# Optimization experiments

Hardware: AMD Instinct MI355X
Metric: run time of the kernel (lower is better)

Reference implementation:

```python
import jax, jax.numpy as jnp
import numpy as np

H = 4096        # hidden_size
NH = 32         # num query heads
NG = 8          # num query groups (kv heads)
HD = H // NH    # head size = 128
B, S = 2, 2048


def gen_rope_cache(seq_length, n_elem, base=10000.0):
    theta = 1.0 / base ** (jnp.arange(0, n_elem, 2, dtype=jnp.float32) / n_elem)
    idx_theta = jnp.outer(jnp.arange(seq_length, dtype=jnp.float32), theta)
    return jnp.stack([jnp.cos(idx_theta), jnp.sin(idx_theta)], axis=-1)  # [S, n_elem//2, 2]


def apply_rope(x, cache):
    # x: [B, S, nh, hd], cache: [S, hd//2, 2]; rot_dim == hd (no pass-through)
    b, s, nh, hd = x.shape
    xr = x.reshape(b, s, nh, hd // 2, 2)
    c = cache[:s].reshape(1, s, 1, hd // 2, 2)
    out = jnp.stack([
        xr[..., 0] * c[..., 0] - xr[..., 1] * c[..., 1],
        xr[..., 1] * c[..., 0] + xr[..., 0] * c[..., 1],
    ], axis=-1)
    return out.reshape(b, s, nh, hd)


def setup_inputs() -> dict:
    key = jax.random.key(0)
    k1, k2, k3, k4 = jax.random.split(key, 4)
    x = jax.random.normal(k1, (B, S, H), dtype=jnp.float32)
    W_qkv = jax.random.normal(k2, (H, H + 2 * NG * HD), dtype=jnp.float32) * 0.02
    b_qkv = jax.random.normal(k3, (H + 2 * NG * HD,), dtype=jnp.float32) * 0.02
    W_dense = jax.random.normal(k4, (H, H), dtype=jnp.float32) * 0.02
    rope_cache = gen_rope_cache(S, HD)
    return {"x": x, "rope_cache": rope_cache, "W_qkv": W_qkv, "b_qkv": b_qkv, "W_dense": W_dense}


def reference(x, rope_cache, W_qkv, b_qkv, W_dense):
    b, s, h = x.shape
    qkv = jnp.einsum('bsh,ho->bso', x, W_qkv) + b_qkv
    q, k, v = jnp.split(qkv, [h, h + NG * HD], axis=-1)
    q = q.reshape(b, s, NH, HD)
    k = k.reshape(b, s, NG, HD)
    v = v.reshape(b, s, NG, HD)
    q = apply_rope(q, rope_cache)
    k = apply_rope(k, rope_cache)
    # GQA: group query heads [B, G, rep, S, D] against kv [B, G, S, D]
    rep = NH // NG
    qg = q.transpose(0, 2, 1, 3).reshape(b, NG, rep, s, HD)
    kg = k.transpose(0, 2, 1, 3)  # [B, G, S, D]
    vg = v.transpose(0, 2, 1, 3)
    scale = 1.0 / jnp.sqrt(jnp.float32(HD))
    scores = jnp.einsum('bgrqd,bgkd->bgrqk', qg, kg) * scale
    causal = jnp.tril(jnp.ones((s, s), dtype=bool))
    scores = jnp.where(causal, scores, jnp.float32(-1e30))
    attn = jax.nn.softmax(scores, axis=-1)
    out = jnp.einsum('bgrqk,bgkd->bgrqd', attn, vg)  # [B, G, rep, S, D]
    out = out.reshape(b, NH, s, HD).transpose(0, 2, 1, 3).reshape(b, s, h)
    return jnp.einsum('bsh,ho->bso', out, W_dense)
```

## Files before the change

kernel.cpp:

```cpp
#include <hip/hip_runtime.h>
#include <hip/hip_bf16.h>
#include <math.h>

#define BS   4096
#define HH   4096
#define NH   32
#define NG   8
#define HD   128
#define SEQ  2048
#define NQKV 6144

typedef float f32x4 __attribute__((ext_vector_type(4)));
typedef float f32x16 __attribute__((ext_vector_type(16)));
typedef short s16x8 __attribute__((ext_vector_type(8)));
typedef short s16x4 __attribute__((ext_vector_type(4)));
typedef unsigned int u32x4 __attribute__((ext_vector_type(4)));

__device__ __forceinline__ unsigned short f2bf(float f) {
  unsigned int u = __builtin_bit_cast(unsigned int, f);
  unsigned int r = (u + 0x7fffu + ((u >> 16) & 1u)) >> 16;
  return (unsigned short)r;
}
__device__ __forceinline__ float b2f(short h) {
  unsigned int u = ((unsigned int)(unsigned short)h) << 16;
  return __builtin_bit_cast(float, u);
}

__device__ __forceinline__ void gload16(const void* g, void* l) {
  __builtin_amdgcn_global_load_lds((__attribute__((address_space(1))) void*)(g),
                                   (__attribute__((address_space(3))) void*)(l), 16, 0, 0);
}

#define BARRIER __builtin_amdgcn_s_barrier()
#define PRIO1 __builtin_amdgcn_s_setprio(1)
#define PRIO0 __builtin_amdgcn_s_setprio(0)

__global__ void cast_f32_bf16(const float* __restrict__ in, short* __restrict__ out, long n4) {
  long i = (long)blockIdx.x * blockDim.x + threadIdx.x;
  long stride = (long)gridDim.x * blockDim.x;
  for (; i < n4; i += stride) {
    float4 v = *(const float4*)&in[i * 4];
    s16x4 o;
    o[0] = (short)f2bf(v.x); o[1] = (short)f2bf(v.y);
    o[2] = (short)f2bf(v.z); o[3] = (short)f2bf(v.w);
    *(s16x4*)&out[i * 4] = o;
  }
}

__global__ __launch_bounds__(256) void transpose_cast(const float* __restrict__ in,
                                                      short* __restrict__ out, int R, int C) {
  __shared__ float tile[32][33];
  int tx = threadIdx.x & 31, ty = threadIdx.x >> 5;
  long c0 = (long)blockIdx.x * 32, r0 = (long)blockIdx.y * 32;
#pragma unroll
  for (int j = 0; j < 32; j += 8)
    tile[ty + j][tx] = in[(r0 + ty + j) * C + c0 + tx];
  __syncthreads();
#pragma unroll
  for (int j = 0; j < 32; j += 8)
    out[(c0 + ty + j) * R + r0 + tx] = (short)f2bf(tile[tx][ty + j]);
}

__global__ __launch_bounds__(256) void transpose_v(const short* __restrict__ in,
                                                   short* __restrict__ out) {
  __shared__ short tile[32][33];
  int tx = threadIdx.x & 31, ty = threadIdx.x >> 5;
  int head = blockIdx.x >> 8;
  int s0 = ((blockIdx.x >> 2) & 63) * 32;
  int d0 = (blockIdx.x & 3) * 32;
  const short* src = in + (long)head * SEQ * HD;
  short* dst = out + (long)head * SEQ * HD;
#pragma unroll
  for (int j = 0; j < 32; j += 8)
    tile[ty + j][tx] = src[(long)(s0 + ty + j) * HD + d0 + tx];
  __syncthreads();
#pragma unroll
  for (int j = 0; j < 32; j += 8)
    dst[(long)(d0 + ty + j) * SEQ + s0 + tx] = tile[tx][ty + j];
}

#define LDA_FR(BASE, DB)                                                         \
  {                                                                              \
    _Pragma("unroll") for (int mf = 0; mf < 4; ++mf)                             \
      _Pragma("unroll") for (int ks = 0; ks < 2; ++ks)                           \
        af[mf][ks] = *(const s16x8*)&lds[(BASE) + (DB) * 8192 + aoff[mf][ks]];   \
  }
#define LDB_FR(BASE, DB)                                                         \
  {                                                                              \
    _Pragma("unroll") for (int nf = 0; nf < 2; ++nf)                             \
      _Pragma("unroll") for (int ks = 0; ks < 2; ++ks)                           \
        bf[nf][ks] = *(const s16x8*)&lds[(BASE) + (DB) * 8192 + boff[nf][ks]];   \
  }
#define MF_Q(MS, NS)                                                             \
  {                                                                              \
    _Pragma("unroll") for (int ks = 0; ks < 2; ++ks)                             \
      _Pragma("unroll") for (int mf = 0; mf < 4; ++mf)                           \
        _Pragma("unroll") for (int nf = 0; nf < 2; ++nf)                         \
          acc[(MS) * 4 + mf][(NS) * 2 + nf] = __builtin_amdgcn_mfma_f32_16x16x32_bf16( \
              af[mf][ks], bf[nf][ks], acc[(MS) * 4 + mf][(NS) * 2 + nf], 0, 0, 0);     \
  }
#define STG_AU0(DB, KB) { gload16(sA0 + (KB), &lds[0 + (DB) * 8192 + du0]);            \
                          gload16(sA1 + (KB), &lds[0 + (DB) * 8192 + du1]); }
#define STG_BU0(DB, KB) { gload16(sB0 + (KB), &lds[32768 + (DB) * 8192 + du0]);        \
                          gload16(sB1 + (KB), &lds[32768 + (DB) * 8192 + du1]); }
#define STG_AU1(DB, KB) { gload16(sA0 + 64 * (long)K + (KB), &lds[16384 + (DB) * 8192 + du0]); \
                          gload16(sA1 + 64 * (long)K + (KB), &lds[16384 + (DB) * 8192 + du1]); }
#define STG_BU1(DB, KB) { gload16(sB0 + 32 * (long)K + (KB), &lds[49152 + (DB) * 8192 + du0]); \
                          gload16(sB1 + 32 * (long)K + (KB), &lds[49152 + (DB) * 8192 + du1]); }

#define TILE256(DB, KBS)                                                         \
  LDA_FR(0, DB); LDB_FR(32768, DB);                                              \
  STG_AU0(DB ^ 1, KBS); STG_BU0(DB ^ 1, KBS);                                    \
  BARRIER;                                                                       \
  PRIO1; MF_Q(0, 0); PRIO0;                                                      \
  asm volatile("s_waitcnt vmcnt(6)" ::: "memory");                               \
  BARRIER;                                                                       \
  LDA_FR(16384, DB);                                                             \
  STG_AU1(DB ^ 1, KBS);                                                          \
  BARRIER;                                                                       \
  PRIO1; MF_Q(1, 0); PRIO0;                                                      \
  asm volatile("s_waitcnt vmcnt(6)" ::: "memory");                               \
  BARRIER;                                                                       \
  LDB_FR(49152, DB);                                                             \
  STG_BU1(DB ^ 1, KBS);                                                          \
  BARRIER;                                                                       \
  PRIO1; MF_Q(1, 1); PRIO0;                                                      \
  BARRIER;                                                                       \
  LDA_FR(0, DB);                                                                 \
  BARRIER;                                                                       \
  PRIO1; MF_Q(0, 1); PRIO0;                                                      \
  asm volatile("s_waitcnt vmcnt(4)" ::: "memory");                               \
  BARRIER;

template <int OUT_BF16, int ADD_BIAS>
__global__ __launch_bounds__(512, 1) void gemm256(const short* __restrict__ A,
                                                  const short* __restrict__ Bt,
                                                  const float* __restrict__ bias,
                                                  void* __restrict__ Cout,
                                                  int M, int N, int K) {
  extern __shared__ short lds[];
  const int t = threadIdx.x;
  const int lane = t & 63, w = t >> 6;
  const int g = lane >> 4, lr = lane & 15;
  const int wm = w >> 2, wn = w & 3;
  const long bm = (long)blockIdx.y * 256;
  const long bn = (long)blockIdx.x * 256;

  const short *sA0, *sA1, *sB0, *sB1;
  {
    int c0 = t, c1 = t + 512;
    int h0 = c0 >> 9, r0 = (c0 >> 3) & 63, tc0 = (c0 & 7) ^ (r0 & 7);
    int h1 = c1 >> 9, r1 = (c1 >> 3) & 63, tc1 = (c1 & 7) ^ (r1 & 7);
    sA0 = A + (bm + h0 * 128 + r0) * (long)K + tc0 * 8;
    sA1 = A + (bm + h1 * 128 + r1) * (long)K + tc1 * 8;
    int g0 = c0 >> 8, rb0 = (c0 >> 3) & 31, tb0 = (c0 & 7) ^ (rb0 & 7);
    int g1 = c1 >> 8, rb1 = (c1 >> 3) & 31, tb1 = (c1 & 7) ^ (rb1 & 7);
    sB0 = Bt + (bn + g0 * 64 + rb0) * (long)K + tb0 * 8;
    sB1 = Bt + (bn + g1 * 64 + rb1) * (long)K + tb1 * 8;
  }
  const int du0 = w * 512;
  const int du1 = w * 512 + 4096;

  int aoff[4][2], boff[2][2];
#pragma unroll
  for (int mf = 0; mf < 4; ++mf)
#pragma unroll
    for (int ks = 0; ks < 2; ++ks)
      aoff[mf][ks] = wm * 4096 + (mf * 16 + lr) * 64 + (((ks * 4 + g) ^ (lr & 7)) * 8);
#pragma unroll
  for (int nf = 0; nf < 2; ++nf)
#pragma unroll
    for (int ks = 0; ks < 2; ++ks)
      boff[nf][ks] = wn * 2048 + (nf * 16 + lr) * 64 + (((ks * 4 + g) ^ (lr & 7)) * 8);

  f32x4 acc[8][4] = {};
  s16x8 af[4][2], bf[2][2];

  STG_AU0(0, 0); STG_BU0(0, 0); STG_AU1(0, 0); STG_BU1(0, 0);
  asm volatile("s_waitcnt vmcnt(0)" ::: "memory");
  BARRIER;

  const int NT = K >> 6;
  for (int kt = 0; kt < NT; kt += 2) {
    const long kb1 = (long)(kt + 1) * 64;
    const long kb2 = (kt + 2 < NT) ? (long)(kt + 2) * 64 : 0l;
    TILE256(0, kb1);
    TILE256(1, kb2);
  }

#pragma unroll
  for (int am = 0; am < 8; ++am) {
    long row = bm + wm * 128 + am * 16 + g * 4;
#pragma unroll
    for (int an = 0; an < 4; ++an) {
      long col = bn + wn * 64 + an * 16 + lr;
      float bv = ADD_BIAS ? bias[col] : 0.0f;
#pragma unroll
      for (int r = 0; r < 4; ++r) {
        float v = acc[am][an][r] + bv;
        if (OUT_BF16) ((short*)Cout)[(row + r) * N + col] = (short)f2bf(v);
        else          ((float*)Cout)[(row + r) * N + col] = v;
      }
    }
  }
}

__global__ void rope_split(const short* __restrict__ qkv, const float* __restrict__ cache,
                           short* __restrict__ Qb, short* __restrict__ Kb,
                           short* __restrict__ Vb) {
  long id = (long)blockIdx.x * blockDim.x + threadIdx.x;
  const long total = (long)BS * (NQKV / 4);
  if (id >= total) return;
  int c4 = (int)(id % (NQKV / 4));
  int row = (int)(id / (NQKV / 4));
  int s = row & (SEQ - 1);
  int b = row >> 11;
  int col = c4 * 4;
  s16x4 in = *(const s16x4*)&qkv[(long)row * NQKV + col];
  if (col < HH) {
    int h = col >> 7, d = col & 127;
    const float4 cs = *(const float4*)&cache[((long)s * 64 + (d >> 1)) * 2];
    float x0 = b2f(in[0]), x1 = b2f(in[1]), x2 = b2f(in[2]), x3 = b2f(in[3]);
    const float sc = 0.12751743f;
    s16x4 o;
    o[0] = (short)f2bf((x0 * cs.x - x1 * cs.y) * sc);
    o[1] = (short)f2bf((x1 * cs.x + x0 * cs.y) * sc);
    o[2] = (short)f2bf((x2 * cs.z - x3 * cs.w) * sc);
    o[3] = (short)f2bf((x3 * cs.z + x2 * cs.w) * sc);
    *(s16x4*)&Qb[(((long)(b * NH + h)) * SEQ + s) * HD + d] = o;
  } else if (col < HH + NG * HD) {
    int cc = col - HH;
    int gi = cc >> 7, d = cc & 127;
    const float4 cs = *(const float4*)&cache[((long)s * 64 + (d >> 1)) * 2];
    float x0 = b2f(in[0]), x1 = b2f(in[1]), x2 = b2f(in[2]), x3 = b2f(in[3]);
    s16x4 o;
    o[0] = (short)f2bf(x0 * cs.x - x1 * cs.y);
    o[1] = (short)f2bf(x1 * cs.x + x0 * cs.y);
    o[2] = (short)f2bf(x2 * cs.z - x3 * cs.w);
    o[3] = (short)f2bf(x3 * cs.z + x2 * cs.w);
    *(s16x4*)&Kb[(((long)(b * NG + gi)) * SEQ + s) * HD + d] = o;
  } else {
    int cc = col - HH - NG * HD;
    int gi = cc >> 7, d = cc & 127;
    *(s16x4*)&Vb[(((long)(b * NG + gi)) * SEQ + s) * HD + d] = in;
  }
}

__global__ __launch_bounds__(512, 1) void attn(const short* __restrict__ Qb,
                                               const short* __restrict__ Kb,
                                               const short* __restrict__ Vtb,
                                               short* __restrict__ Ob) {
  extern __shared__ short alds[];
  const int t = threadIdx.x, lane = t & 63, w = t >> 6;
  const int l31 = lane & 31, hi = lane >> 5;
  const int qt = 7 - (int)(blockIdx.x >> 6);
  const int head = blockIdx.x & 63;
  const int b = head >> 5, h = head & 31;
  const int qb = qt * 256;
  const short* Qhead = Qb + (long)(b * NH + h) * SEQ * HD;
  const short* Khead = Kb + (long)(b * NG + (h >> 2)) * SEQ * HD;
  const short* Vthead = Vtb + (long)(b * NG + (h >> 2)) * SEQ * HD;
  const int qw0 = qb + w * 32;
  const int qrow = qw0 + l31;
  float* facs = (float*)&alds[32768] + w * 32;

  s16x8 qf[8];
#pragma unroll
  for (int ds = 0; ds < 8; ++ds)
    qf[ds] = *(const s16x8*)&Qhead[(long)qrow * HD + ds * 16 + hi * 8];

  const short *kp0, *kp1, *vp0, *vp1;
  {
    int c0 = t, c1 = t + 512;
    int kr0 = c0 >> 4, kc0 = (c0 & 15) ^ (kr0 & 15);
    int kr1 = c1 >> 4, kc1 = (c1 & 15) ^ (kr1 & 15);
    kp0 = Khead + (long)kr0 * HD + kc0 * 8;
    kp1 = Khead + (long)kr1 * HD + kc1 * 8;
    int vr0 = c0 >> 3, vc0 = (c0 & 7) ^ (vr0 & 7);
    int vr1 = c1 >> 3, vc1 = (c1 & 7) ^ (vr1 & 7);
    vp0 = Vthead + (long)vr0 * SEQ + vc0 * 8;
    vp1 = Vthead + (long)vr1 * SEQ + vc1 * 8;
  }
  const int d0 = w * 512, d1 = w * 512 + 4096;

  f32x16 ao[4] = {};
  float mrun = -1.0e30f, lrun = 0.0f;
  const int nkt = 4 * qt + 4;

  gload16(kp0, &alds[d0]); gload16(kp1, &alds[d1]);
  gload16(vp0, &alds[16384 + d0]); gload16(vp1, &alds[16384 + d1]);
  kp0 += 64 * HD; kp1 += 64 * HD; vp0 += 64; vp1 += 64;
  asm volatile("s_waitcnt vmcnt(0)" ::: "memory");
  BARRIER;

  for (int kt = 0; kt < nkt; ++kt) {
    const int buf = kt & 1, nb = buf ^ 1;
    const int kb = kt * 64;
    const int bK = buf * 8192, bV = 16384 + buf * 8192;
    if (kt + 1 < nkt) {
      gload16(kp0, &alds[nb * 8192 + d0]); gload16(kp1, &alds[nb * 8192 + d1]);
      gload16(vp0, &alds[16384 + nb * 8192 + d0]); gload16(vp1, &alds[16384 + nb * 8192 + d1]);
      kp0 += 64 * HD; kp1 += 64 * HD; vp0 += 64; vp1 += 64;
    }
    if (kb <= qw0 + 31) {
      f32x16 st0 = {}, st1 = {};
      PRIO1;
#pragma unroll
      for (int ds = 0; ds < 8; ++ds) {
        const int c = ds * 2 + hi;
        const int r0 = l31, r1 = 32 + l31;
        s16x8 kf0 = *(const s16x8*)&alds[bK + r0 * 128 + ((c ^ (r0 & 15)) * 8)];
        s16x8 kf1 = *(const s16x8*)&alds[bK + r1 * 128 + ((c ^ (r1 & 15)) * 8)];
        st0 = __builtin_amdgcn_mfma_f32_32x32x16_bf16(kf0, qf[ds], st0, 0, 0, 0);
        st1 = __builtin_amdgcn_mfma_f32_32x32x16_bf16(kf1, qf[ds], st1, 0, 0, 0);
      }
      PRIO0;

      float p[32];
      if (kb + 63 > qrow || kb + 63 > qw0) {
#pragma unroll
        for (int r = 0; r < 16; ++r) {
          int kg = kb + (r & 3) + 8 * (r >> 2) + 4 * hi;
          p[r] = (kg > qrow) ? -1.0e30f : st0[r];
          p[16 + r] = (kg + 32 > qrow) ? -1.0e30f : st1[r];
        }
      } else {
#pragma unroll
        for (int r = 0; r < 16; ++r) { p[r] = st0[r]; p[16 + r] = st1[r]; }
      }
      float tmax = -1.0e30f;
#pragma unroll
      for (int i = 0; i < 32; ++i) tmax = fmaxf(tmax, p[i]);
      tmax = fmaxf(tmax, __shfl_xor(tmax, 32));
      if (!__all(tmax <= mrun + 8.0f)) {
        float mnew = fmaxf(mrun, tmax);
        float fac = exp2f(mrun - mnew);
        facs[l31] = fac;
        mrun = mnew; lrun *= fac;
        f32x4 f0 = *(f32x4*)&facs[0 + 4 * hi];
        f32x4 f1 = *(f32x4*)&facs[8 + 4 * hi];
        f32x4 f2 = *(f32x4*)&facs[16 + 4 * hi];
        f32x4 f3 = *(f32x4*)&facs[24 + 4 * hi];
#pragma unroll
        for (int j = 0; j < 4; ++j)
#pragma unroll
          for (int dt = 0; dt < 4; ++dt) {
            ao[dt][j] *= f0[j]; ao[dt][4 + j] *= f1[j];
            ao[dt][8 + j] *= f2[j]; ao[dt][12 + j] *= f3[j];
          }
      }
      float tsum = 0.0f;
#pragma unroll
      for (int i = 0; i < 32; ++i) { p[i] = exp2f(p[i] - mrun); tsum += p[i]; }
      lrun += tsum + __shfl_xor(tsum, 32);

      s16x8 pa[4];
#pragma unroll
      for (int ks = 0; ks < 4; ++ks) {
        unsigned w0, w1, w2, w3;
        asm("v_cvt_pk_bf16_f32 %0, %1, %2" : "=v"(w0) : "v"(p[ks * 8 + 0]), "v"(p[ks * 8 + 1]));
        asm("v_cvt_pk_bf16_f32 %0, %1, %2" : "=v"(w1) : "v"(p[ks * 8 + 2]), "v"(p[ks * 8 + 3]));
        asm("v_cvt_pk_bf16_f32 %0, %1, %2" : "=v"(w2) : "v"(p[ks * 8 + 4]), "v"(p[ks * 8 + 5]));
        asm("v_cvt_pk_bf16_f32 %0, %1, %2" : "=v"(w3) : "v"(p[ks * 8 + 6]), "v"(p[ks * 8 + 7]));
        unsigned sw0 = (unsigned)__shfl_xor((int)w0, 32);
        unsigned sw1 = (unsigned)__shfl_xor((int)w1, 32);
        unsigned sw2 = (unsigned)__shfl_xor((int)w2, 32);
        unsigned sw3 = (unsigned)__shfl_xor((int)w3, 32);
        u32x4 pw;
        pw[0] = hi ? sw2 : w0;
        pw[1] = hi ? sw3 : w1;
        pw[2] = hi ? w2 : sw0;
        pw[3] = hi ? w3 : sw1;
        pa[ks] = __builtin_bit_cast(s16x8, pw);
      }

      PRIO1;
#pragma unroll
      for (int ks = 0; ks < 4; ++ks)
#pragma unroll
        for (int dt = 0; dt < 4; ++dt) {
          int dd = dt * 32 + l31;
          int slot = (ks * 2 + hi) ^ (dd & 7);
          s16x8 vf = *(const s16x8*)&alds[bV + dd * 64 + slot * 8];
          ao[dt] = __builtin_amdgcn_mfma_f32_32x32x16_bf16(pa[ks], vf, ao[dt], 0, 0, 0);
        }
      PRIO0;
    }
    asm volatile("s_waitcnt vmcnt(0)" ::: "memory");
    BARRIER;
  }

  facs[l31] = 1.0f / lrun;
  float invr[16];
  {
    f32x4 i0 = *(f32x4*)&facs[0 + 4 * hi];
    f32x4 i1 = *(f32x4*)&facs[8 + 4 * hi];
    f32x4 i2 = *(f32x4*)&facs[16 + 4 * hi];
    f32x4 i3 = *(f32x4*)&facs[24 + 4 * hi];
#pragma unroll
    for (int j = 0; j < 4; ++j) {
      invr[j] = i0[j]; invr[4 + j] = i1[j]; invr[8 + j] = i2[j]; invr[12 + j] = i3[j];
    }
  }
#pragma unroll
  for (int dt = 0; dt < 4; ++dt)
#pragma unroll
    for (int r = 0; r < 16; ++r) {
      int grow = qw0 + (r & 3) + 8 * (r >> 2) + 4 * hi;
      Ob[((long)b * SEQ + grow) * HH + h * HD + dt * 32 + l31] = (short)f2bf(ao[dt][r] * invr[r]);
    }
}

extern "C" void kernel_launch(void* const* d_in, const int* in_sizes, int n_in,
                              void* d_out, int out_size, void* d_ws, size_t ws_size,
                              hipStream_t stream) {
  const float* x     = (const float*)d_in[0];
  const float* cache = (const float*)d_in[1];
  const float* Wqkv  = (const float*)d_in[2];
  const float* bqkv  = (const float*)d_in[3];
  const float* Wd    = (const float*)d_in[4];

  char* ws = (char*)d_ws;
  short* xb   = (short*)(ws);
  short* wqt  = (short*)(ws + 33554432ll);
  short* wdt  = (short*)(ws + 83886080ll);
  short* qkvb = (short*)(ws + 117440512ll);
  short* Qb   = (short*)(ws + 167772160ll);
  short* Kb   = (short*)(ws + 201326592ll);
  short* Vb   = (short*)(ws + 209715200ll);
  short* Vtb  = (short*)(ws + 218103808ll);
  short* Ob   = (short*)(ws + 226492416ll);

  cast_f32_bf16<<<2048, 256, 0, stream>>>(x, xb, (long)BS * HH / 4);
  transpose_cast<<<dim3(NQKV / 32, HH / 32), 256, 0, stream>>>(Wqkv, wqt, HH, NQKV);
  transpose_cast<<<dim3(HH / 32, HH / 32), 256, 0, stream>>>(Wd, wdt, HH, HH);
  gemm256<1, 1><<<dim3(NQKV / 256, BS / 256), 512, 131072, stream>>>(xb, wqt, bqkv, qkvb, BS, NQKV, HH);
  rope_split<<<(int)(((long)BS * (NQKV / 4) + 255) / 256), 256, 0, stream>>>(qkvb, cache, Qb, Kb, Vb);
  transpose_v<<<16 * 64 * 4, 256, 0, stream>>>(Vb, Vtb);
  attn<<<512, 512, 66560, stream>>>(Qb, Kb, Vtb, Ob);
  gemm256<0, 0><<<dim3(HH / 256, BS / 256), 512, 131072, stream>>>(Ob, wdt, nullptr, d_out, BS, HH, HH);
}
```

Measured before the change: 534.1 us.

## Fuse bias, RoPE, head split and V transpose into QKV GEMM epilogue

The QKV GEMM epilogue now adds the bias, applies RoPE to Q and K using a lane shuffle to fetch each pair partner, scales Q, and writes Q, K and transposed V directly in attention layout. This removes the rope_split and transpose_v kernels and the bf16 qkv intermediate round trip through memory. The TILE256 macro also reorders its sub-tile MFMA and LDS fragment load sequence so B fragments are reused differently. The new epilogue issues scattered 2-byte stores for Q and K and extra cache loads per element, which may be less coalesced than before.

Measured after the change: 517.4 us. 1.03x faster.

```diff
diff --git a/kernel.cpp b/kernel.cpp
--- a/kernel.cpp
+++ b/kernel.cpp
@@ -61,24 +61,6 @@
     out[(c0 + ty + j) * R + r0 + tx] = (short)f2bf(tile[tx][ty + j]);
 }
 
-__global__ __launch_bounds__(256) void transpose_v(const short* __restrict__ in,
-                                                   short* __restrict__ out) {
-  __shared__ short tile[32][33];
-  int tx = threadIdx.x & 31, ty = threadIdx.x >> 5;
-  int head = blockIdx.x >> 8;
-  int s0 = ((blockIdx.x >> 2) & 63) * 32;
-  int d0 = (blockIdx.x & 3) * 32;
-  const short* src = in + (long)head * SEQ * HD;
-  short* dst = out + (long)head * SEQ * HD;
-#pragma unroll
-  for (int j = 0; j < 32; j += 8)
-    tile[ty + j][tx] = src[(long)(s0 + ty + j) * HD + d0 + tx];
-  __syncthreads();
-#pragma unroll
-  for (int j = 0; j < 32; j += 8)
-    dst[(long)(d0 + ty + j) * SEQ + s0 + tx] = tile[tx][ty + j];
-}
-
 #define LDA_FR(BASE, DB)                                                         \
   {                                                                              \
     _Pragma("unroll") for (int mf = 0; mf < 4; ++mf)                             \
@@ -115,28 +97,32 @@
   PRIO1; MF_Q(0, 0); PRIO0;                                                      \
   asm volatile("s_waitcnt vmcnt(6)" ::: "memory");                               \
   BARRIER;                                                                       \
+  LDB_FR(49152, DB);                                                             \
+  STG_BU1(DB ^ 1, KBS);                                                          \
+  BARRIER;                                                                       \
+  PRIO1; MF_Q(0, 1); PRIO0;                                                      \
+  asm volatile("s_waitcnt vmcnt(6)" ::: "memory");                               \
+  BARRIER;                                                                       \
   LDA_FR(16384, DB);                                                             \
   STG_AU1(DB ^ 1, KBS);                                                          \
   BARRIER;                                                                       \
+  PRIO1; MF_Q(1, 1); PRIO0;                                                      \
+  BARRIER;                                                                       \
+  LDB_FR(32768, DB);                                                             \
+  BARRIER;                                                                       \
   PRIO1; MF_Q(1, 0); PRIO0;                                                      \
-  asm volatile("s_waitcnt vmcnt(6)" ::: "memory");                               \
-  BARRIER;                                                                       \
-  LDB_FR(49152, DB);                                                             \
-  STG_BU1(DB ^ 1, KBS);                                                          \
-  BARRIER;                                                                       \
-  PRIO1; MF_Q(1, 1); PRIO0;                                                      \
-  BARRIER;                                                                       \
-  LDA_FR(0, DB);                                                                 \
-  BARRIER;                                                                       \
-  PRIO1; MF_Q(0, 1); PRIO0;                                                      \
   asm volatile("s_waitcnt vmcnt(4)" ::: "memory");                               \
   BARRIER;
 
-template <int OUT_BF16, int ADD_BIAS>
+template <int MODE>
 __global__ __launch_bounds__(512, 1) void gemm256(const short* __restrict__ A,
                                                   const short* __restrict__ Bt,
                                                   const float* __restrict__ bias,
                                                   void* __restrict__ Cout,
+                                                  const float* __restrict__ cache,
+                                                  short* __restrict__ Qb,
+                                                  short* __restrict__ Kb,
+                                                  short* __restrict__ Vtb,
                                                   int M, int N, int K) {
   extern __shared__ short lds[];
   const int t = threadIdx.x;
@@ -188,61 +174,62 @@
     TILE256(1, kb2);
   }
 
-#pragma unroll
-  for (int am = 0; am < 8; ++am) {
-    long row = bm + wm * 128 + am * 16 + g * 4;
-#pragma unroll
-    for (int an = 0; an < 4; ++an) {
-      long col = bn + wn * 64 + an * 16 + lr;
-      float bv = ADD_BIAS ? bias[col] : 0.0f;
-#pragma unroll
-      for (int r = 0; r < 4; ++r) {
-        float v = acc[am][an][r] + bv;
-        if (OUT_BF16) ((short*)Cout)[(row + r) * N + col] = (short)f2bf(v);
-        else          ((float*)Cout)[(row + r) * N + col] = v;
-      }
-    }
-  }
-}
-
-__global__ void rope_split(const short* __restrict__ qkv, const float* __restrict__ cache,
-                           short* __restrict__ Qb, short* __restrict__ Kb,
-                           short* __restrict__ Vb) {
-  long id = (long)blockIdx.x * blockDim.x + threadIdx.x;
-  const long total = (long)BS * (NQKV / 4);
-  if (id >= total) return;
-  int c4 = (int)(id % (NQKV / 4));
-  int row = (int)(id / (NQKV / 4));
-  int s = row & (SEQ - 1);
-  int b = row >> 11;
-  int col = c4 * 4;
-  s16x4 in = *(const s16x4*)&qkv[(long)row * NQKV + col];
-  if (col < HH) {
-    int h = col >> 7, d = col & 127;
-    const float4 cs = *(const float4*)&cache[((long)s * 64 + (d >> 1)) * 2];
-    float x0 = b2f(in[0]), x1 = b2f(in[1]), x2 = b2f(in[2]), x3 = b2f(in[3]);
-    const float sc = 0.12751743f;
-    s16x4 o;
-    o[0] = (short)f2bf((x0 * cs.x - x1 * cs.y) * sc);
-    o[1] = (short)f2bf((x1 * cs.x + x0 * cs.y) * sc);
-    o[2] = (short)f2bf((x2 * cs.z - x3 * cs.w) * sc);
-    o[3] = (short)f2bf((x3 * cs.z + x2 * cs.w) * sc);
-    *(s16x4*)&Qb[(((long)(b * NH + h)) * SEQ + s) * HD + d] = o;
-  } else if (col < HH + NG * HD) {
-    int cc = col - HH;
-    int gi = cc >> 7, d = cc & 127;
-    const float4 cs = *(const float4*)&cache[((long)s * 64 + (d >> 1)) * 2];
-    float x0 = b2f(in[0]), x1 = b2f(in[1]), x2 = b2f(in[2]), x3 = b2f(in[3]);
-    s16x4 o;
-    o[0] = (short)f2bf(x0 * cs.x - x1 * cs.y);
-    o[1] = (short)f2bf(x1 * cs.x + x0 * cs.y);
-    o[2] = (short)f2bf(x2 * cs.z - x3 * cs.w);
-    o[3] = (short)f2bf(x3 * cs.z + x2 * cs.w);
-    *(s16x4*)&Kb[(((long)(b * NG + gi)) * SEQ + s) * HD + d] = o;
+  if (MODE == 0) {
+#pragma unroll
+    for (int am = 0; am < 8; ++am) {
+      long row = bm + wm * 128 + am * 16 + g * 4;
+#pragma unroll
+      for (int an = 0; an < 4; ++an) {
+        long col = bn + wn * 64 + an * 16 + lr;
+#pragma unroll
+        for (int r = 0; r < 4; ++r)
+          ((float*)Cout)[(row + r) * N + col] = acc[am][an][r];
+      }
+    }
   } else {
-    int cc = col - HH - NG * HD;
-    int gi = cc >> 7, d = cc & 127;
-    *(s16x4*)&Vb[(((long)(b * NG + gi)) * SEQ + s) * HD + d] = in;
+    const float scq = 0.12751743f;
+#pragma unroll
+    for (int am = 0; am < 8; ++am) {
+      int row0 = (int)bm + wm * 128 + am * 16 + g * 4;
+      int s0 = row0 & (SEQ - 1);
+      int bb = row0 >> 11;
+#pragma unroll
+      for (int an = 0; an < 4; ++an) {
+        int col = (int)bn + wn * 64 + an * 16 + lr;
+        float bv = bias[col];
+        if (col < HH) {
+          int h = col >> 7, d = col & 127;
+          const int odd = lr & 1;
+#pragma unroll
+          for (int r = 0; r < 4; ++r) {
+            float v = acc[am][an][r] + bv;
+            float p = __shfl_xor(v, 1);
+            float2 cs = *(const float2*)&cache[((long)(s0 + r) * 64 + (d >> 1)) * 2];
+            float o = odd ? (v * cs.x + p * cs.y) : (v * cs.x - p * cs.y);
+            Qb[((long)(bb * NH + h) * SEQ + s0 + r) * HD + d] = (short)f2bf(o * scq);
+          }
+        } else if (col < HH + NG * HD) {
+          int cc = col - HH;
+          int gi = cc >> 7, d = cc & 127;
+          const int odd = lr & 1;
+#pragma unroll
+          for (int r = 0; r < 4; ++r) {
+            float v = acc[am][an][r] + bv;
+            float p = __shfl_xor(v, 1);
+            float2 cs = *(const float2*)&cache[((long)(s0 + r) * 64 + (d >> 1)) * 2];
+            float o = odd ? (v * cs.x + p * cs.y) : (v * cs.x - p * cs.y);
+            Kb[((long)(bb * NG + gi) * SEQ + s0 + r) * HD + d] = (short)f2bf(o);
+          }
+        } else {
+          int cc = col - HH - NG * HD;
+          int gi = cc >> 7, d = cc & 127;
+          s16x4 o;
+#pragma unroll
+          for (int r = 0; r < 4; ++r) o[r] = (short)f2bf(acc[am][an][r] + bv);
+          *(s16x4*)&Vtb[((long)(bb * NG + gi) * HD + d) * SEQ + s0] = o;
+        }
+      }
+    }
   }
 }
 
@@ -424,19 +411,17 @@
   short* xb   = (short*)(ws);
   short* wqt  = (short*)(ws + 33554432ll);
   short* wdt  = (short*)(ws + 83886080ll);
-  short* qkvb = (short*)(ws + 117440512ll);
   short* Qb   = (short*)(ws + 167772160ll);
   short* Kb   = (short*)(ws + 201326592ll);
-  short* Vb   = (short*)(ws + 209715200ll);
   short* Vtb  = (short*)(ws + 218103808ll);
   short* Ob   = (short*)(ws + 226492416ll);
 
   cast_f32_bf16<<<2048, 256, 0, stream>>>(x, xb, (long)BS * HH / 4);
   transpose_cast<<<dim3(NQKV / 32, HH / 32), 256, 0, stream>>>(Wqkv, wqt, HH, NQKV);
   transpose_cast<<<dim3(HH / 32, HH / 32), 256, 0, stream>>>(Wd, wdt, HH, HH);
-  gemm256<1, 1><<<dim3(NQKV / 256, BS / 256), 512, 131072, stream>>>(xb, wqt, bqkv, qkvb, BS, NQKV, HH);
-  rope_split<<<(int)(((long)BS * (NQKV / 4) + 255) / 256), 256, 0, stream>>>(qkvb, cache, Qb, Kb, Vb);
-  transpose_v<<<16 * 64 * 4, 256, 0, stream>>>(Vb, Vtb);
+  gemm256<2><<<dim3(NQKV / 256, BS / 256), 512, 131072, stream>>>(
+      xb, wqt, bqkv, nullptr, cache, Qb, Kb, Vtb, BS, NQKV, HH);
   attn<<<512, 512, 66560, stream>>>(Qb, Kb, Vtb, Ob);
-  gemm256<0, 0><<<dim3(HH / 256, BS / 256), 512, 131072, stream>>>(Ob, wdt, nullptr, d_out, BS, HH, HH);
-}
+  gemm256<0><<<dim3(HH / 256, BS / 256), 512, 131072, stream>>>(
+      Ob, wdt, nullptr, d_out, nullptr, nullptr, nullptr, nullptr, BS, HH, HH);
+}
```
